# Performance work log

Measured on AMD Instinct MI355X. Metric: run time of the kernel, lower is better.

## Reference

```python
import jax, jax.numpy as jnp
import numpy as np


def setup_inputs() -> dict:
    key = jax.random.key(0)
    k1, k2 = jax.random.split(key)
    B, OUT_DIM, S = 4, 1024, 2048
    IN_DIM = 4096
    x = jax.random.normal(k1, (B, OUT_DIM, S), dtype=jnp.float32)
    w = jax.random.normal(k2, (IN_DIM, OUT_DIM), dtype=jnp.float32) * 0.02
    return {"x": x, "w": w}


def reference(x, w):
    # Original: mse[b,i,s] = mean_o (w[i,o] - x[b,o,s])^2
    # Computed via the squared-distance expansion to avoid the
    # (B, in_dim, S, out_dim) broadcast intermediate:
    #   mean_o (w-x)^2 = (||w||^2 - 2 w.x + ||x||^2) / out_dim
    out_dim = w.shape[1]
    w2 = jnp.sum(w * w, axis=1)[None, :, None]            # (1, in_dim, 1)
    x2 = jnp.sum(x * x, axis=1)[:, None, :]               # (B, 1, S)
    wx = jnp.einsum('io,bos->bis', w, x)                  # (B, in_dim, S)
    return (w2 - 2.0 * wx + x2) / out_dim
```

## Files before the change

kernel.cpp:

```cpp
#include <hip/hip_runtime.h>
#include <stdint.h>


#define M_DIM 4096
#define K_DIM 1024
#define N_DIM 2048
#define B_DIM 4
#define NF 8192

#define BM 256
#define BN 256
#define BK 128
#define NKT (K_DIM / BK)
#define MT (M_DIM / BM)
#define NT (NF / BN)
#define BUFB 65536

typedef __attribute__((ext_vector_type(4))) int i32x4;
typedef __attribute__((ext_vector_type(8))) int i32x8;
typedef __attribute__((ext_vector_type(4))) float f32x4;
typedef __attribute__((ext_vector_type(4))) float f32x4v;

__global__ __launch_bounds__(256) void prep_all(const float* __restrict__ w,
                                                const float* __restrict__ x,
                                                uint8_t* __restrict__ w8,
                                                uint8_t* __restrict__ x8,
                                                float* __restrict__ w2,
                                                float* __restrict__ x2) {
  __shared__ uint8_t tile[64][68];
  __shared__ float red[4];
  const int bid = blockIdx.x;
  const int t = threadIdx.x;

  if (bid < M_DIM) {
    const int i = bid;
    f32x4v v =
        __builtin_nontemporal_load(((const f32x4v*)(w + (size_t)i * K_DIM)) + t);
    float ss = v.x * v.x + v.y * v.y + v.z * v.z + v.w * v.w;
    uint32_t pk = 0;
    pk = __builtin_amdgcn_cvt_pk_fp8_f32(v.x * 64.0f, v.y * 64.0f, pk, false);
    pk = __builtin_amdgcn_cvt_pk_fp8_f32(v.z * 64.0f, v.w * 64.0f, pk, true);
    ((uint32_t*)(w8 + (size_t)i * K_DIM))[t] = pk;
#pragma unroll
    for (int off = 32; off > 0; off >>= 1) ss += __shfl_down(ss, off);
    if ((t & 63) == 0) red[t >> 6] = ss;
    __syncthreads();
    if (t == 0) w2[i] = red[0] + red[1] + red[2] + red[3];
    return;
  }

  const int idx = bid - M_DIM;
  const int s0 = (idx & 31) * 64;
  const int o0 = ((idx >> 5) & 15) * 64;
  const int b = idx >> 9;
  const int tr = t >> 4;
  const int tc = t & 15;
  float ss0 = 0, ss1 = 0, ss2 = 0, ss3 = 0;
#pragma unroll
  for (int p = 0; p < 4; ++p) {
    const int r = p * 16 + tr;
    f32x4v v = __builtin_nontemporal_load(
        ((const f32x4v*)(x + ((size_t)(b * K_DIM + o0 + r)) * N_DIM + s0)) + tc);
    ss0 += v.x * v.x; ss1 += v.y * v.y; ss2 += v.z * v.z; ss3 += v.w * v.w;
    uint32_t pk = 0;
    pk = __builtin_amdgcn_cvt_pk_fp8_f32(v.x, v.y, pk, false);
    pk = __builtin_amdgcn_cvt_pk_fp8_f32(v.z, v.w, pk, true);
    *(uint32_t*)&tile[r][tc * 4] = pk;
  }
  ss0 += __shfl_xor(ss0, 16); ss0 += __shfl_xor(ss0, 32);
  ss1 += __shfl_xor(ss1, 16); ss1 += __shfl_xor(ss1, 32);
  ss2 += __shfl_xor(ss2, 16); ss2 += __shfl_xor(ss2, 32);
  ss3 += __shfl_xor(ss3, 16); ss3 += __shfl_xor(ss3, 32);
  if ((t & 63) < 16) {
    float* xp = x2 + b * N_DIM + s0 + tc * 4;
    atomicAdd(xp + 0, ss0);
    atomicAdd(xp + 1, ss1);
    atomicAdd(xp + 2, ss2);
    atomicAdd(xp + 3, ss3);
  }
  __syncthreads();
#pragma unroll
  for (int p = 0; p < 4; ++p) {
    const int s = p * 16 + tr;
    const int a = tc * 4;
    uint32_t o = (uint32_t)tile[a][s] | ((uint32_t)tile[a + 1][s] << 8) |
                 ((uint32_t)tile[a + 2][s] << 16) | ((uint32_t)tile[a + 3][s] << 24);
    *(uint32_t*)(x8 + ((size_t)(b * N_DIM + s0 + s)) * K_DIM + o0 + a) = o;
  }
}

typedef const __attribute__((address_space(1))) uint32_t* gp_t;
typedef __attribute__((address_space(3))) uint32_t* lp_t;

__device__ __forceinline__ void gload_lds16(const void* g, const void* l) {
  __builtin_amdgcn_global_load_lds((gp_t)(uintptr_t)g,
                                   (lp_t)(uint32_t)(uintptr_t)l, 16, 0, 0);
}

#define MFMA8(a, b, c) \
  __builtin_amdgcn_mfma_scale_f32_16x16x128_f8f6f4((a), (b), (c), 0, 0, 0, 127, 0, 127)
#define FENCE() asm volatile("" ::: "memory")

__global__ __launch_bounds__(512) void gemm_mse8(
    const uint8_t* __restrict__ w8, const uint8_t* __restrict__ x8,
    const float* __restrict__ w2, const float* __restrict__ x2,
    float* __restrict__ out) {
  __shared__ __align__(32) char smem[2 * BUFB];
  const int tid = threadIdx.x;
  const int wid = tid >> 6;
  const int lane = tid & 63;
  const int laneR = lane & 15;
  const int g = lane >> 4;
  const int wm = wid >> 2;
  const int wn = wid & 3;

  const int bid = blockIdx.x;
  const int xcd = bid & 7;
  const int r = bid >> 3;
  const int st = r >> 4;
  const int sub = r & 15;
  const int mt = st * 4 + (sub & 3);
  const int nt = xcd * 4 + (sub >> 2);

  const uint8_t* Ag = w8 + (size_t)mt * BM * K_DIM;
  const uint8_t* Bg = x8 + (size_t)nt * BN * K_DIM;

#define SRCOFF(P) ((size_t)((P) >> 7) * K_DIM + (((P) ^ ((((P) >> 7) & 7) << 4)) & 127))
  const int p0 = tid * 16;
  const uint8_t* sA0 = Ag + SRCOFF(p0);
  const uint8_t* sA1 = Ag + SRCOFF(p0 + 8192);
  const uint8_t* sA2 = Ag + SRCOFF(p0 + 16384);
  const uint8_t* sA3 = Ag + SRCOFF(p0 + 24576);
  const uint8_t* sB0 = Bg + SRCOFF(p0);
  const uint8_t* sB1 = Bg + SRCOFF(p0 + 8192);
  const uint8_t* sB2 = Bg + SRCOFF(p0 + 16384);
  const uint8_t* sB3 = Bg + SRCOFF(p0 + 24576);

#define STAGE(tt, buf)                                   \
  {                                                      \
    const int ko_ = (tt) * BK;                           \
    char* lb_ = smem + (buf) * BUFB;                     \
    gload_lds16(sA0 + ko_, lb_ + p0);                    \
    gload_lds16(sA1 + ko_, lb_ + p0 + 8192);             \
    gload_lds16(sA2 + ko_, lb_ + p0 + 16384);            \
    gload_lds16(sA3 + ko_, lb_ + p0 + 24576);            \
    gload_lds16(sB0 + ko_, lb_ + 32768 + p0);            \
    gload_lds16(sB1 + ko_, lb_ + 32768 + p0 + 8192);     \
    gload_lds16(sB2 + ko_, lb_ + 32768 + p0 + 16384);    \
    gload_lds16(sB3 + ko_, lb_ + 32768 + p0 + 24576);    \
  }

  const int tail = (g << 5) ^ ((laneR & 7) << 4);
  const int offA0 = (wm * 128 + laneR) * 128 + tail;
  const int offB0 = 32768 + (wn * 64 + laneR) * 128 + tail;

#define LDF(off, bo)                                                          \
  ({                                                                          \
    i32x4 lo_ = *(const i32x4*)(smem + (bo) + (off));                         \
    i32x4 hi_ = *(const i32x4*)(smem + (bo) + ((off) ^ 16));                  \
    (i32x8){lo_[0], lo_[1], lo_[2], lo_[3], hi_[0], hi_[1], hi_[2], hi_[3]};  \
  })

  f32x4 acc[8][4] = {};

  STAGE(0, 0);
  asm volatile("s_waitcnt vmcnt(0)" ::: "memory");
  __builtin_amdgcn_s_barrier();
  FENCE();

#pragma unroll
  for (int t = 0; t < NKT; ++t) {
    const int bo = (t & 1) * BUFB;
    if (t < NKT - 1) STAGE(t + 1, (t + 1) & 1);
    i32x8 b0 = LDF(offB0 + 0 * 2048, bo);
    i32x8 b1 = LDF(offB0 + 1 * 2048, bo);
    i32x8 b2 = LDF(offB0 + 2 * 2048, bo);
    i32x8 b3 = LDF(offB0 + 3 * 2048, bo);
    __builtin_amdgcn_s_setprio(1);
#pragma unroll
    for (int mi = 0; mi < 8; ++mi) {
      i32x8 am = LDF(offA0 + mi * 2048, bo);
      acc[mi][0] = MFMA8(am, b0, acc[mi][0]);
      acc[mi][1] = MFMA8(am, b1, acc[mi][1]);
      acc[mi][2] = MFMA8(am, b2, acc[mi][2]);
      acc[mi][3] = MFMA8(am, b3, acc[mi][3]);
    }
    __builtin_amdgcn_s_setprio(0);
    asm volatile("s_waitcnt vmcnt(0)" ::: "memory");
    asm volatile("s_waitcnt lgkmcnt(0)" ::: "memory");
    __builtin_amdgcn_sched_barrier(0);
    __builtin_amdgcn_s_barrier();
    FENCE();
  }

  const float cA = 0.03125f;
  const float inv = 1.0f / (float)K_DIM;
  const int rowb0 = mt * BM + wm * 128;
  const int colf0 = nt * BN + wn * 64;
  const int bz = colf0 >> 11;
  const int sc0 = colf0 & (N_DIM - 1);
  float xv[4];
#pragma unroll
  for (int ni = 0; ni < 4; ++ni) xv[ni] = x2[colf0 + ni * 16 + laneR];
  float* lds_f = (float*)smem + wid * 4096;
  float* outp = out + (size_t)bz * M_DIM * N_DIM;

#pragma unroll
  for (int miH = 0; miH < 2; ++miH) {
#pragma unroll
    for (int mi4 = 0; mi4 < 4; ++mi4) {
      const int mi = miH * 4 + mi4;
#pragma unroll
      for (int j = 0; j < 4; ++j) {
        const int r2 = mi4 * 16 + g * 4 + j;
        const float wv = w2[rowb0 + miH * 64 + r2];
#pragma unroll
        for (int ni = 0; ni < 4; ++ni) {
          const int c = ni * 16 + laneR;
          lds_f[r2 * 64 + (c ^ ((r2 & 7) << 2))] =
              (wv + xv[ni] - acc[mi][ni][j] * cA) * inv;
        }
      }
    }
#pragma unroll
    for (int k = 0; k < 16; ++k) {
      const int r2 = k * 4 + (lane >> 4);
      const int c0 = laneR * 4;
      f32x4 v = *(const f32x4*)&lds_f[r2 * 64 + (c0 ^ ((r2 & 7) << 2))];
      *(f32x4*)(outp + (size_t)(rowb0 + miH * 64 + r2) * N_DIM + sc0 + c0) = v;
    }
    asm volatile("s_waitcnt lgkmcnt(0)" ::: "memory");
  }
#undef STAGE
#undef LDF
#undef SRCOFF
}

extern "C" void kernel_launch(void* const* d_in, const int* in_sizes, int n_in,
                              void* d_out, int out_size, void* d_ws, size_t ws_size,
                              hipStream_t stream) {
  const float* x = (const float*)d_in[0];
  const float* w = (const float*)d_in[1];
  float* out = (float*)d_out;
  char* ws = (char*)d_ws;
  uint8_t* w8 = (uint8_t*)ws;
  uint8_t* x8 = (uint8_t*)(ws + (size_t)(4 << 20));
  float* w2 = (float*)(ws + (size_t)(12 << 20));
  float* x2 = w2 + M_DIM;

  (void)hipMemsetAsync(x2, 0, NF * sizeof(float), stream);
  prep_all<<<dim3(M_DIM + 2048), dim3(256), 0, stream>>>(w, x, w8, x8, w2, x2);
  gemm_mse8<<<dim3(MT * NT), dim3(512), 0, stream>>>(w8, x8, w2, x2, out);
}
```

Baseline: 81.85 us.

## Quantize GEMM operands to FP4 e2m1 instead of FP8

The prep kernel now quantizes w (pre-scaled) and x into packed 4-bit e2m1 codes, using a threshold-based encoder, instead of FP8. The GEMM loads half as many bytes per K-tile with 4 K-tiles instead of 8. It issues scaled MFMA with the FP4 format selector, where each instruction consumes 128 K elements from 64 bytes. The intent is to halve operand bandwidth and LDS traffic and to use the higher FP4 matrix throughput. The cost is much coarser quantization of the dot-product term, which risks accuracy, and slower scalar byte-wise encoding in the prep kernel.

```diff
diff --git a/kernel.cpp b/kernel.cpp
--- a/kernel.cpp
+++ b/kernel.cpp
@@ -10,8 +10,7 @@
 
 #define BM 256
 #define BN 256
-#define BK 128
-#define NKT (K_DIM / BK)
+#define NKT 4
 #define MT (M_DIM / BM)
 #define NT (NF / BN)
 #define BUFB 65536
@@ -21,10 +20,18 @@
 typedef __attribute__((ext_vector_type(4))) float f32x4;
 typedef __attribute__((ext_vector_type(4))) float f32x4v;
 
+__device__ __forceinline__ uint32_t fp4q(float a) {
+  uint32_t s = (__float_as_uint(a) >> 31) << 3;
+  float t = fabsf(a);
+  int idx = (t > 0.25f) + (t > 0.75f) + (t > 1.25f) + (t > 1.75f) +
+            (t > 2.5f) + (t > 3.5f) + (t > 5.0f);
+  return s | (uint32_t)idx;
+}
+
 __global__ __launch_bounds__(256) void prep_all(const float* __restrict__ w,
                                                 const float* __restrict__ x,
-                                                uint8_t* __restrict__ w8,
-                                                uint8_t* __restrict__ x8,
+                                                uint8_t* __restrict__ w4,
+                                                uint8_t* __restrict__ x4,
                                                 float* __restrict__ w2,
                                                 float* __restrict__ x2) {
   __shared__ uint8_t tile[64][68];
@@ -37,10 +44,9 @@
     f32x4v v =
         __builtin_nontemporal_load(((const f32x4v*)(w + (size_t)i * K_DIM)) + t);
     float ss = v.x * v.x + v.y * v.y + v.z * v.z + v.w * v.w;
-    uint32_t pk = 0;
-    pk = __builtin_amdgcn_cvt_pk_fp8_f32(v.x * 64.0f, v.y * 64.0f, pk, false);
-    pk = __builtin_amdgcn_cvt_pk_fp8_f32(v.z * 64.0f, v.w * 64.0f, pk, true);
-    ((uint32_t*)(w8 + (size_t)i * K_DIM))[t] = pk;
+    ushort pk = (ushort)(fp4q(v.x * 64.0f) | (fp4q(v.y * 64.0f) << 4) |
+                         (fp4q(v.z * 64.0f) << 8) | (fp4q(v.w * 64.0f) << 12));
+    ((ushort*)(w4 + (size_t)i * 512))[t] = pk;
 #pragma unroll
     for (int off = 32; off > 0; off >>= 1) ss += __shfl_down(ss, off);
     if ((t & 63) == 0) red[t >> 6] = ss;
@@ -62,10 +68,10 @@
     f32x4v v = __builtin_nontemporal_load(
         ((const f32x4v*)(x + ((size_t)(b * K_DIM + o0 + r)) * N_DIM + s0)) + tc);
     ss0 += v.x * v.x; ss1 += v.y * v.y; ss2 += v.z * v.z; ss3 += v.w * v.w;
-    uint32_t pk = 0;
-    pk = __builtin_amdgcn_cvt_pk_fp8_f32(v.x, v.y, pk, false);
-    pk = __builtin_amdgcn_cvt_pk_fp8_f32(v.z, v.w, pk, true);
-    *(uint32_t*)&tile[r][tc * 4] = pk;
+    tile[r][tc * 4 + 0] = (uint8_t)fp4q(v.x);
+    tile[r][tc * 4 + 1] = (uint8_t)fp4q(v.y);
+    tile[r][tc * 4 + 2] = (uint8_t)fp4q(v.z);
+    tile[r][tc * 4 + 3] = (uint8_t)fp4q(v.w);
   }
   ss0 += __shfl_xor(ss0, 16); ss0 += __shfl_xor(ss0, 32);
   ss1 += __shfl_xor(ss1, 16); ss1 += __shfl_xor(ss1, 32);
@@ -82,10 +88,11 @@
 #pragma unroll
   for (int p = 0; p < 4; ++p) {
     const int s = p * 16 + tr;
+    const int sF = b * N_DIM + s0 + s;
     const int a = tc * 4;
-    uint32_t o = (uint32_t)tile[a][s] | ((uint32_t)tile[a + 1][s] << 8) |
-                 ((uint32_t)tile[a + 2][s] << 16) | ((uint32_t)tile[a + 3][s] << 24);
-    *(uint32_t*)(x8 + ((size_t)(b * N_DIM + s0 + s)) * K_DIM + o0 + a) = o;
+    ushort bb = (ushort)(tile[a][s] | (tile[a + 1][s] << 4) |
+                         (tile[a + 2][s] << 8) | (tile[a + 3][s] << 12));
+    ((ushort*)(x4 + (size_t)sF * 512 + (o0 >> 1)))[tc] = bb;
   }
 }
 
@@ -97,12 +104,16 @@
                                    (lp_t)(uint32_t)(uintptr_t)l, 16, 0, 0);
 }
 
-#define MFMA8(a, b, c) \
-  __builtin_amdgcn_mfma_scale_f32_16x16x128_f8f6f4((a), (b), (c), 0, 0, 0, 127, 0, 127)
+__device__ __forceinline__ f32x4 mfma4(i32x4 a, i32x4 b, f32x4 c) {
+  i32x8 a8 = {a[0], a[1], a[2], a[3], 0, 0, 0, 0};
+  i32x8 b8 = {b[0], b[1], b[2], b[3], 0, 0, 0, 0};
+  return __builtin_amdgcn_mfma_scale_f32_16x16x128_f8f6f4(a8, b8, c, 4, 4, 0,
+                                                          127, 0, 127);
+}
 #define FENCE() asm volatile("" ::: "memory")
 
-__global__ __launch_bounds__(512) void gemm_mse8(
-    const uint8_t* __restrict__ w8, const uint8_t* __restrict__ x8,
+__global__ __launch_bounds__(512) void gemm_mse4(
+    const uint8_t* __restrict__ w4, const uint8_t* __restrict__ x4,
     const float* __restrict__ w2, const float* __restrict__ x2,
     float* __restrict__ out) {
   __shared__ __align__(32) char smem[2 * BUFB];
@@ -122,10 +133,10 @@
   const int mt = st * 4 + (sub & 3);
   const int nt = xcd * 4 + (sub >> 2);
 
-  const uint8_t* Ag = w8 + (size_t)mt * BM * K_DIM;
-  const uint8_t* Bg = x8 + (size_t)nt * BN * K_DIM;
-
-#define SRCOFF(P) ((size_t)((P) >> 7) * K_DIM + (((P) ^ ((((P) >> 7) & 7) << 4)) & 127))
+  const uint8_t* Ag = w4 + (size_t)mt * BM * 512;
+  const uint8_t* Bg = x4 + (size_t)nt * BN * 512;
+
+#define SRCOFF(P) ((size_t)((P) >> 7) * 512 + (((P) ^ ((((P) >> 7) & 7) << 4)) & 127))
   const int p0 = tid * 16;
   const uint8_t* sA0 = Ag + SRCOFF(p0);
   const uint8_t* sA1 = Ag + SRCOFF(p0 + 8192);
@@ -138,7 +149,7 @@
 
 #define STAGE(tt, buf)                                   \
   {                                                      \
-    const int ko_ = (tt) * BK;                           \
+    const int ko_ = (tt) * 128;                          \
     char* lb_ = smem + (buf) * BUFB;                     \
     gload_lds16(sA0 + ko_, lb_ + p0);                    \
     gload_lds16(sA1 + ko_, lb_ + p0 + 8192);             \
@@ -150,16 +161,13 @@
     gload_lds16(sB3 + ko_, lb_ + 32768 + p0 + 24576);    \
   }
 
-  const int tail = (g << 5) ^ ((laneR & 7) << 4);
-  const int offA0 = (wm * 128 + laneR) * 128 + tail;
-  const int offB0 = 32768 + (wn * 64 + laneR) * 128 + tail;
-
-#define LDF(off, bo)                                                          \
-  ({                                                                          \
-    i32x4 lo_ = *(const i32x4*)(smem + (bo) + (off));                         \
-    i32x4 hi_ = *(const i32x4*)(smem + (bo) + ((off) ^ 16));                  \
-    (i32x8){lo_[0], lo_[1], lo_[2], lo_[3], hi_[0], hi_[1], hi_[2], hi_[3]};  \
-  })
+  const int swz = (laneR & 7) << 4;
+  const int t0 = (g << 4) ^ swz;
+  const int t1 = (64 | (g << 4)) ^ swz;
+  const int offA_ = (wm * 128 + laneR) * 128;
+  const int offB_ = 32768 + (wn * 64 + laneR) * 128;
+
+#define LDF4(off, bo) (*(const i32x4*)(smem + (bo) + (off)))
 
   f32x4 acc[8][4] = {};
 
@@ -172,18 +180,27 @@
   for (int t = 0; t < NKT; ++t) {
     const int bo = (t & 1) * BUFB;
     if (t < NKT - 1) STAGE(t + 1, (t + 1) & 1);
-    i32x8 b0 = LDF(offB0 + 0 * 2048, bo);
-    i32x8 b1 = LDF(offB0 + 1 * 2048, bo);
-    i32x8 b2 = LDF(offB0 + 2 * 2048, bo);
-    i32x8 b3 = LDF(offB0 + 3 * 2048, bo);
+    i32x4 b00 = LDF4(offB_ + 0 * 2048 + t0, bo);
+    i32x4 b10 = LDF4(offB_ + 1 * 2048 + t0, bo);
+    i32x4 b20 = LDF4(offB_ + 2 * 2048 + t0, bo);
+    i32x4 b30 = LDF4(offB_ + 3 * 2048 + t0, bo);
+    i32x4 b01 = LDF4(offB_ + 0 * 2048 + t1, bo);
+    i32x4 b11 = LDF4(offB_ + 1 * 2048 + t1, bo);
+    i32x4 b21 = LDF4(offB_ + 2 * 2048 + t1, bo);
+    i32x4 b31 = LDF4(offB_ + 3 * 2048 + t1, bo);
     __builtin_amdgcn_s_setprio(1);
 #pragma unroll
     for (int mi = 0; mi < 8; ++mi) {
-      i32x8 am = LDF(offA0 + mi * 2048, bo);
-      acc[mi][0] = MFMA8(am, b0, acc[mi][0]);
-      acc[mi][1] = MFMA8(am, b1, acc[mi][1]);
-      acc[mi][2] = MFMA8(am, b2, acc[mi][2]);
-      acc[mi][3] = MFMA8(am, b3, acc[mi][3]);
+      i32x4 a0 = LDF4(offA_ + mi * 2048 + t0, bo);
+      acc[mi][0] = mfma4(a0, b00, acc[mi][0]);
+      acc[mi][1] = mfma4(a0, b10, acc[mi][1]);
+      acc[mi][2] = mfma4(a0, b20, acc[mi][2]);
+      acc[mi][3] = mfma4(a0, b30, acc[mi][3]);
+      i32x4 a1 = LDF4(offA_ + mi * 2048 + t1, bo);
+      acc[mi][0] = mfma4(a1, b01, acc[mi][0]);
+      acc[mi][1] = mfma4(a1, b11, acc[mi][1]);
+      acc[mi][2] = mfma4(a1, b21, acc[mi][2]);
+      acc[mi][3] = mfma4(a1, b31, acc[mi][3]);
     }
     __builtin_amdgcn_s_setprio(0);
     asm volatile("s_waitcnt vmcnt(0)" ::: "memory");
@@ -232,7 +249,7 @@
     asm volatile("s_waitcnt lgkmcnt(0)" ::: "memory");
   }
 #undef STAGE
-#undef LDF
+#undef LDF4
 #undef SRCOFF
 }
 
@@ -243,12 +260,12 @@
   const float* w = (const float*)d_in[1];
   float* out = (float*)d_out;
   char* ws = (char*)d_ws;
-  uint8_t* w8 = (uint8_t*)ws;
-  uint8_t* x8 = (uint8_t*)(ws + (size_t)(4 << 20));
-  float* w2 = (float*)(ws + (size_t)(12 << 20));
+  uint8_t* w4 = (uint8_t*)ws;
+  uint8_t* x4 = (uint8_t*)(ws + (size_t)(2 << 20));
+  float* w2 = (float*)(ws + (size_t)(8 << 20));
   float* x2 = w2 + M_DIM;
 
   (void)hipMemsetAsync(x2, 0, NF * sizeof(float), stream);
-  prep_all<<<dim3(M_DIM + 2048), dim3(256), 0, stream>>>(w, x, w8, x8, w2, x2);
-  gemm_mse8<<<dim3(MT * NT), dim3(512), 0, stream>>>(w8, x8, w2, x2, out);
-}
+  prep_all<<<dim3(M_DIM + 2048), dim3(256), 0, stream>>>(w, x, w4, x4, w2, x2);
+  gemm_mse4<<<dim3(MT * NT), dim3(512), 0, stream>>>(w4, x4, w2, x2, out);
+}
```

New measurement: 71.40 us. 1.15x faster.
